# Optimization experiments

Hardware: AMD Instinct MI355X
Metric: run time of the kernel (lower is better)

## Reference

```python
import jax, jax.numpy as jnp
import numpy as np

B, S, D = 2, 2048, 2048
H, KV, HD = 8, 1, 256          # num_heads, num_kv_heads, head_dim
ROPE_BASE = 10000.0
NEG_INF = -1e9


def _rope_cos_sin(position_ids, head_dim, base):
    # position_ids: [B, S] -> cos/sin: [B, S, head_dim]
    inv_freq = 1.0 / (base ** (jnp.arange(0, head_dim, 2, dtype=jnp.float32) / head_dim))
    freqs = position_ids.astype(jnp.float32)[..., None] * inv_freq  # [B,S,HD/2]
    emb = jnp.concatenate([freqs, freqs], axis=-1)                  # [B,S,HD]
    return jnp.cos(emb), jnp.sin(emb)


def _rotate_half(x):
    h = x.shape[-1] // 2
    return jnp.concatenate([-x[..., h:], x[..., :h]], axis=-1)


def _apply_rope(x, cos, sin):
    # x: [B,h,S,HD]; cos/sin: [B,S,HD]
    c = cos[:, None, :, :]
    s = sin[:, None, :, :]
    return x * c + _rotate_half(x) * s


def setup_inputs() -> dict:
    key = jax.random.key(0)
    ks = jax.random.split(key, 6)
    hidden_state = jax.random.normal(ks[0], (B, S, D), dtype=jnp.float32)
    # additive causal mask: 0 on/below diagonal, -inf above
    causal = jnp.tril(jnp.ones((S, S), dtype=bool))
    attention_mask = jnp.where(causal, 0.0, NEG_INF).astype(jnp.float32)[None, None]  # [B?1,1,S,S]
    attention_mask = jnp.broadcast_to(attention_mask, (B, 1, S, S))
    position_ids = jnp.broadcast_to(jnp.arange(S, dtype=jnp.int64)[None, :], (B, S))
    scale = 0.02
    Wq = jax.random.normal(ks[1], (D, H * HD), dtype=jnp.float32) * scale
    Wk = jax.random.normal(ks[2], (D, KV * HD), dtype=jnp.float32) * scale
    Wv = jax.random.normal(ks[3], (D, KV * HD), dtype=jnp.float32) * scale
    Wo = jax.random.normal(ks[4], (H * HD, D), dtype=jnp.float32) * scale
    return {"hidden_state": hidden_state, "attention_mask": attention_mask,
            "position_ids": position_ids, "Wq": Wq, "Wk": Wk, "Wv": Wv, "Wo": Wo}


def reference(hidden_state, attention_mask, position_ids, Wq, Wk, Wv, Wo):
    bsz, q_len, _ = hidden_state.shape
    n_rep = H // KV
    # projections
    q = (hidden_state @ Wq).reshape(bsz, q_len, H, HD).transpose(0, 2, 1, 3)   # [B,H,S,HD]
    k = (hidden_state @ Wk).reshape(bsz, q_len, KV, HD).transpose(0, 2, 1, 3)  # [B,KV,S,HD]
    v = (hidden_state @ Wv).reshape(bsz, q_len, KV, HD).transpose(0, 2, 1, 3)
    # RoPE
    cos, sin = _rope_cos_sin(position_ids, HD, ROPE_BASE)
    q = _apply_rope(q, cos, sin)
    k = _apply_rope(k, cos, sin)
    # GQA: repeat kv heads
    k = jnp.repeat(k, n_rep, axis=1)  # [B,H,S,HD]
    v = jnp.repeat(v, n_rep, axis=1)
    # eager attention with full score matrix (faithful to source)
    scores = jnp.einsum('bhqd,bhkd->bhqk', q, k) / jnp.sqrt(jnp.float32(HD))
    scores = scores + attention_mask
    attn = jax.nn.softmax(scores.astype(jnp.float32), axis=-1).astype(q.dtype)
    out = jnp.einsum('bhqk,bhkd->bhqd', attn, v)            # [B,H,S,HD]
    out = out.transpose(0, 2, 1, 3).reshape(bsz, q_len, H * HD)
    return out @ Wo
```

## Files before the change

kernel.cpp:

```cpp
#include <hip/hip_runtime.h>
#include <cstdint>
#include <cstddef>

#define B_   2
#define S_   2048
#define D_   2048
#define H_   8
#define HD_  256
#define M_   (B_ * S_)
#define NQ_  (H_ * HD_)
#define NKV_ 256

typedef unsigned short u16;
typedef __attribute__((ext_vector_type(8))) short short8v;
typedef __attribute__((ext_vector_type(4))) float f32x4;

__device__ __forceinline__ u16 f2bf_rn(float x) {
    unsigned int u = __float_as_uint(x);
    unsigned int r = u + 0x7FFFu + ((u >> 16) & 1u);
    return (u16)(r >> 16);
}
__device__ __forceinline__ float bf2f(u16 h) {
    return __uint_as_float(((unsigned int)h) << 16);
}

__device__ __forceinline__ void gll16(const u16* g, u16* l) {
    __builtin_amdgcn_global_load_lds(
        (const __attribute__((address_space(1))) void*)(g),
        (__attribute__((address_space(3))) void*)(l), 16, 0, 0);
}

__global__ __launch_bounds__(256) void split_kernel(const float* __restrict__ in,
                                                    u16* __restrict__ hi,
                                                    u16* __restrict__ lo)
{
    const size_t i = ((size_t)blockIdx.x * 256 + threadIdx.x) * 8;
    float4 v0 = *(const float4*)(in + i);
    float4 v1 = *(const float4*)(in + i + 4);
    float xs[8] = {v0.x, v0.y, v0.z, v0.w, v1.x, v1.y, v1.z, v1.w};
    unsigned int hv[4], lv[4];
#pragma unroll
    for (int k = 0; k < 4; ++k) {
        u16 h0 = f2bf_rn(xs[2 * k]);
        u16 h1 = f2bf_rn(xs[2 * k + 1]);
        u16 l0 = f2bf_rn(xs[2 * k] - bf2f(h0));
        u16 l1 = f2bf_rn(xs[2 * k + 1] - bf2f(h1));
        hv[k] = (unsigned int)h0 | ((unsigned int)h1 << 16);
        lv[k] = (unsigned int)l0 | ((unsigned int)l1 << 16);
    }
    *(uint4*)(hi + i) = make_uint4(hv[0], hv[1], hv[2], hv[3]);
    *(uint4*)(lo + i) = make_uint4(lv[0], lv[1], lv[2], lv[3]);
}

__global__ __launch_bounds__(256) void tsplit_kernel(const float* __restrict__ W,
                                                     u16* __restrict__ Th,
                                                     u16* __restrict__ Tl,
                                                     int K, int N)
{
    __shared__ float t[64][65];
    const int kt = blockIdx.x, nt = blockIdx.y;
    const int c4 = (threadIdx.x & 15) * 4;
    const int r  = threadIdx.x >> 4;

#pragma unroll
    for (int s = 0; s < 4; ++s) {
        const int kk = r + s * 16;
        float4 v = *(const float4*)(W + (size_t)(kt * 64 + kk) * N + nt * 64 + c4);
        t[kk][c4 + 0] = v.x;
        t[kk][c4 + 1] = v.y;
        t[kk][c4 + 2] = v.z;
        t[kk][c4 + 3] = v.w;
    }
    __syncthreads();
#pragma unroll
    for (int s = 0; s < 4; ++s) {
        const int nn = r + s * 16;
        unsigned int hv[2], lv[2];
#pragma unroll
        for (int p = 0; p < 2; ++p) {
            u16 h0, h1, l0, l1;
            float x0 = t[c4 + 2 * p][nn];
            float x1 = t[c4 + 2 * p + 1][nn];
            h0 = f2bf_rn(x0); l0 = f2bf_rn(x0 - bf2f(h0));
            h1 = f2bf_rn(x1); l1 = f2bf_rn(x1 - bf2f(h1));
            hv[p] = (unsigned int)h0 | ((unsigned int)h1 << 16);
            lv[p] = (unsigned int)l0 | ((unsigned int)l1 << 16);
        }
        u16* ph = Th + (size_t)(nt * 64 + nn) * K + kt * 64 + c4;
        u16* pl = Tl + (size_t)(nt * 64 + nn) * K + kt * 64 + c4;
        *(uint2*)ph = make_uint2(hv[0], hv[1]);
        *(uint2*)pl = make_uint2(lv[0], lv[1]);
    }
}

__device__ __forceinline__ void mfma_gemm_tile(
    const u16* __restrict__ Ah, const u16* __restrict__ Al,
    const u16* __restrict__ Bh, const u16* __restrict__ Bl,
    float* __restrict__ C, const int Kd, const int ldc,
    const int bm0, const int bn0)
{
    __shared__ u16 ldsAh[128 * 32];
    __shared__ u16 ldsAl[128 * 32];
    __shared__ u16 ldsBh[128 * 32];
    __shared__ u16 ldsBl[128 * 32];

    const int tid  = threadIdx.x;
    const int lane = tid & 63;
    const int w    = tid >> 6;
    const int wr   = w >> 1, wc = w & 1;

    const int srow = w * 32 + (lane >> 2);
    const int schk = (lane & 3) * 8;
    const u16* gAh = Ah + (size_t)(bm0 + srow) * Kd + schk;
    const u16* gAl = Al + (size_t)(bm0 + srow) * Kd + schk;
    const u16* gBh = Bh + (size_t)(bn0 + srow) * Kd + schk;
    const u16* gBl = Bl + (size_t)(bn0 + srow) * Kd + schk;

    f32x4 acc[4][4];
#pragma unroll
    for (int i = 0; i < 4; ++i)
#pragma unroll
        for (int j = 0; j < 4; ++j) acc[i][j] = (f32x4){0.f, 0.f, 0.f, 0.f};

    const int fr = lane & 15;
    const int kb = (lane >> 4) * 8;

    for (int k0 = 0; k0 < Kd; k0 += 32) {
        if (k0) __syncthreads();
#pragma unroll
        for (int c = 0; c < 2; ++c) {
            const size_t go = (size_t)(c * 16) * Kd + k0;
            const int lb = (w * 32 + c * 16) * 32;
            gll16(gAh + go, &ldsAh[lb]);
            gll16(gAl + go, &ldsAl[lb]);
            gll16(gBh + go, &ldsBh[lb]);
            gll16(gBl + go, &ldsBl[lb]);
        }
        __syncthreads();

        short8v a_h[4], a_l[4], b_h[4], b_l[4];
#pragma unroll
        for (int f = 0; f < 4; ++f) {
            const int ra = (wr * 64 + f * 16 + fr) * 32 + kb;
            const int rb = (wc * 64 + f * 16 + fr) * 32 + kb;
            a_h[f] = *(const short8v*)&ldsAh[ra];
            a_l[f] = *(const short8v*)&ldsAl[ra];
            b_h[f] = *(const short8v*)&ldsBh[rb];
            b_l[f] = *(const short8v*)&ldsBl[rb];
        }
#pragma unroll
        for (int i = 0; i < 4; ++i)
#pragma unroll
            for (int j = 0; j < 4; ++j) {
                acc[i][j] = __builtin_amdgcn_mfma_f32_16x16x32_bf16(a_h[i], b_h[j], acc[i][j], 0, 0, 0);
                acc[i][j] = __builtin_amdgcn_mfma_f32_16x16x32_bf16(a_h[i], b_l[j], acc[i][j], 0, 0, 0);
                acc[i][j] = __builtin_amdgcn_mfma_f32_16x16x32_bf16(a_l[i], b_h[j], acc[i][j], 0, 0, 0);
            }
    }

    const int cr = (lane >> 4) * 4;
    const int cc = lane & 15;
#pragma unroll
    for (int i = 0; i < 4; ++i)
#pragma unroll
        for (int j = 0; j < 4; ++j) {
#pragma unroll
            for (int r = 0; r < 4; ++r) {
                C[(size_t)(bm0 + wr * 64 + i * 16 + cr + r) * ldc
                  + (bn0 + wc * 64 + j * 16 + cc)] = acc[i][j][r];
            }
        }
}

__global__ __launch_bounds__(256, 2) void qkv_mfma_kernel(
    const u16* __restrict__ Xh, const u16* __restrict__ Xl,
    const u16* __restrict__ WqTh, const u16* __restrict__ WqTl,
    const u16* __restrict__ WkTh, const u16* __restrict__ WkTl,
    const u16* __restrict__ WvTh, const u16* __restrict__ WvTl,
    float* __restrict__ Qo, float* __restrict__ Ko, float* __restrict__ Vo)
{
    const int bn = blockIdx.x;
    const u16 *Bh, *Bl; float* C; int ldc, col0;
    if (bn < 16)      { Bh = WqTh; Bl = WqTl; C = Qo; ldc = NQ_;  col0 = bn * 128; }
    else if (bn < 18) { Bh = WkTh; Bl = WkTl; C = Ko; ldc = NKV_; col0 = (bn - 16) * 128; }
    else              { Bh = WvTh; Bl = WvTl; C = Vo; ldc = NKV_; col0 = (bn - 18) * 128; }
    mfma_gemm_tile(Xh, Xl, Bh, Bl, C, D_, ldc, blockIdx.y * 128, col0);
}

__global__ __launch_bounds__(256, 2) void out_mfma_kernel(
    const u16* __restrict__ Ch, const u16* __restrict__ Cl,
    const u16* __restrict__ WoTh, const u16* __restrict__ WoTl,
    float* __restrict__ Out)
{
    mfma_gemm_tile(Ch, Cl, WoTh, WoTl, Out, NQ_, D_, blockIdx.y * 128, blockIdx.x * 128);
}

__global__ __launch_bounds__(128) void rope_split_q_kernel(
    const float* __restrict__ Qw, u16* __restrict__ Qh, u16* __restrict__ Ql)
{
    const int row = blockIdx.x;
    const int d = threadIdx.x;
    const int s = row & (S_ - 1);

    const float expo = (float)(2 * d) / (float)HD_;
    const float inv_freq = 1.0f / powf(10000.0f, expo);
    float sn, c;
    sincosf((float)s * inv_freq, &sn, &c);

    const float* qr = Qw + (size_t)row * NQ_;
    u16* qhr = Qh + (size_t)row * NQ_;
    u16* qlr = Ql + (size_t)row * NQ_;
#pragma unroll
    for (int h = 0; h < H_; ++h) {
        float x0 = qr[h * HD_ + d];
        float x1 = qr[h * HD_ + d + 128];
        float y0 = x0 * c - x1 * sn;
        float y1 = x1 * c + x0 * sn;
        u16 h0 = f2bf_rn(y0), h1 = f2bf_rn(y1);
        qhr[h * HD_ + d]       = h0;
        qhr[h * HD_ + d + 128] = h1;
        qlr[h * HD_ + d]       = f2bf_rn(y0 - bf2f(h0));
        qlr[h * HD_ + d + 128] = f2bf_rn(y1 - bf2f(h1));
    }
}

__global__ __launch_bounds__(128) void rope_split_k_swz_kernel(
    const float* __restrict__ Kw, u16* __restrict__ Kh, u16* __restrict__ Kl)
{
    const int row = blockIdx.x;
    const int d = threadIdx.x;
    const int s = row & (S_ - 1);
    const int xm = row & 7;

    const float expo = (float)(2 * d) / (float)HD_;
    const float inv_freq = 1.0f / powf(10000.0f, expo);
    float sn, c;
    sincosf((float)s * inv_freq, &sn, &c);

    const float* kr = Kw + (size_t)row * HD_;
    float x0 = kr[d], x1 = kr[d + 128];
    float y0 = x0 * c - x1 * sn;
    float y1 = x1 * c + x0 * sn;
    u16 h0 = f2bf_rn(y0), h1 = f2bf_rn(y1);

    const int o0 = (((d >> 3) ^ xm) << 3) | (d & 7);
    const int o1 = ((((d + 128) >> 3) ^ xm) << 3) | (d & 7);
    Kh[(size_t)row * HD_ + o0] = h0;
    Kh[(size_t)row * HD_ + o1] = h1;
    Kl[(size_t)row * HD_ + o0] = f2bf_rn(y0 - bf2f(h0));
    Kl[(size_t)row * HD_ + o1] = f2bf_rn(y1 - bf2f(h1));
}

#define KVB_ 32
#define PBS_ 44

__global__ __launch_bounds__(256, 2) void attn_mfma_kernel(
    const u16* __restrict__ Qh, const u16* __restrict__ Ql,
    const u16* __restrict__ Kh, const u16* __restrict__ Kl,
    const u16* __restrict__ VtH, const u16* __restrict__ VtL,
    float* __restrict__ O)
{
    __shared__ u16 kvK[2 * 32 * 256];
    __shared__ u16 kvV[2 * 256 * 32];
    __shared__ u16 pb[2 * 64 * PBS_];

    const int tid = threadIdx.x;
    const int lane = tid & 63;
    const int w = tid >> 6;

    const int u = blockIdx.x & 255;
    const int pair = blockIdx.x >> 8;
    const int qt_base = u & 31;
    const int qt = pair ? (31 - qt_base) : qt_base;
    const int bh = (u >> 5) + pair * 8;
    const int b = bh >> 3, h = bh & 7;

    const int fr = lane & 15;
    const int kq = (lane >> 4);
    const int xm = fr & 7;

    short8v qfh[8], qfl[8];
    {
        const size_t qrow = (size_t)(b * S_ + qt * 64 + w * 16 + fr);
        const u16* ph = Qh + qrow * NQ_ + h * HD_ + kq * 8;
        const u16* pl = Ql + qrow * NQ_ + h * HD_ + kq * 8;
#pragma unroll
        for (int ks = 0; ks < 8; ++ks) {
            qfh[ks] = *(const short8v*)(ph + ks * 32);
            qfl[ks] = *(const short8v*)(pl + ks * 32);
        }
    }

    f32x4 oacc[16];
#pragma unroll
    for (int f = 0; f < 16; ++f) oacc[f] = (f32x4){0.f, 0.f, 0.f, 0.f};
    float m_i[4] = {-1e30f, -1e30f, -1e30f, -1e30f};
    float l_i[4] = {0.f, 0.f, 0.f, 0.f};

    const u16* ksrc[2] = {Kh + (size_t)b * S_ * HD_, Kl + (size_t)b * S_ * HD_};
    const u16* vsrc[2] = {VtH + (size_t)b * HD_ * S_, VtL + (size_t)b * HD_ * S_};

    const int k_rl = w * 8 + (lane >> 5) * 0;
    const int k_hi = (lane >> 5);
    const int k_ch = lane & 31;
    const int v_dl = w * 64 + (lane >> 2);
    const int v_cc = (lane & 3) * 8;

    const int nkt = (qt + 1) * 2;

#define STAGE_K(KT)                                                            \
    {                                                                          \
        _Pragma("unroll")                                                      \
        for (int c = 0; c < 2; ++c) {                                          \
            _Pragma("unroll")                                                  \
            for (int t = 0; t < 4; ++t) {                                      \
                const int rl = k_rl + t * 2 + k_hi;                            \
                gll16(ksrc[c] + (size_t)((KT) * KVB_ + rl) * HD_ + k_ch * 8,   \
                      &kvK[c * 8192 + (w * 2048 + t * 512)]);                  \
            }                                                                  \
        }                                                                      \
    }

#define STAGE_V(KT)                                                            \
    {                                                                          \
        _Pragma("unroll")                                                      \
        for (int c = 0; c < 2; ++c) {                                          \
            _Pragma("unroll")                                                  \
            for (int t = 0; t < 4; ++t) {                                      \
                gll16(vsrc[c] + (size_t)(v_dl + t * 16) * S_ + (KT) * KVB_ + v_cc, \
                      &kvV[c * 8192 + (w * 2048 + t * 512)]);                  \
            }                                                                  \
        }                                                                      \
    }

    STAGE_K(0)
    STAGE_V(0)
    __syncthreads();

    for (int kt = 0; kt < nkt; ++kt) {
        const bool more = (kt + 1 < nkt);

        f32x4 s0 = (f32x4){0.f, 0.f, 0.f, 0.f};
        f32x4 s1 = (f32x4){0.f, 0.f, 0.f, 0.f};
#pragma unroll
        for (int ks = 0; ks < 8; ++ks) {
            const int ch = (ks * 4 + kq) ^ xm;
            short8v kh0 = *(const short8v*)&kvK[fr * 256 + ch * 8];
            short8v kh1 = *(const short8v*)&kvK[(16 + fr) * 256 + ch * 8];
            short8v kl0 = *(const short8v*)&kvK[8192 + fr * 256 + ch * 8];
            short8v kl1 = *(const short8v*)&kvK[8192 + (16 + fr) * 256 + ch * 8];
            s0 = __builtin_amdgcn_mfma_f32_16x16x32_bf16(qfh[ks], kh0, s0, 0, 0, 0);
            s1 = __builtin_amdgcn_mfma_f32_16x16x32_bf16(qfh[ks], kh1, s1, 0, 0, 0);
            s0 = __builtin_amdgcn_mfma_f32_16x16x32_bf16(qfh[ks], kl0, s0, 0, 0, 0);
            s1 = __builtin_amdgcn_mfma_f32_16x16x32_bf16(qfh[ks], kl1, s1, 0, 0, 0);
            s0 = __builtin_amdgcn_mfma_f32_16x16x32_bf16(qfl[ks], kh0, s0, 0, 0, 0);
            s1 = __builtin_amdgcn_mfma_f32_16x16x32_bf16(qfl[ks], kh1, s1, 0, 0, 0);
        }

        const int qglob = qt * 64 + w * 16 + kq * 4;
        const int kg = kt * KVB_ + fr;
        float mxv[4];
        bool need = false;
#pragma unroll
        for (int r = 0; r < 4; ++r) {
            float x0 = s0[r] * 0.0625f;
            float x1 = s1[r] * 0.0625f;
            if (kg > qglob + r)      x0 = -1e30f;
            if (kg + 16 > qglob + r) x1 = -1e30f;
            s0[r] = x0; s1[r] = x1;
            float mx = fmaxf(x0, x1);
#pragma unroll
            for (int off = 1; off < 16; off <<= 1)
                mx = fmaxf(mx, __shfl_xor(mx, off, 64));
            mxv[r] = mx;
            need = need || (mx > m_i[r] + 8.0f);
        }
        if (__any((int)need)) {
#pragma unroll
            for (int r = 0; r < 4; ++r) {
                const float mnew = fmaxf(m_i[r], mxv[r]);
                const float alpha = __expf(m_i[r] - mnew);
                l_i[r] *= alpha;
                m_i[r] = mnew;
#pragma unroll
                for (int f = 0; f < 16; ++f) oacc[f][r] *= alpha;
            }
        }
#pragma unroll
        for (int r = 0; r < 4; ++r) {
            const float p0 = __expf(s0[r] - m_i[r]);
            const float p1 = __expf(s1[r] - m_i[r]);
            float ps = p0 + p1;
#pragma unroll
            for (int off = 1; off < 16; off <<= 1)
                ps += __shfl_xor(ps, off, 64);
            l_i[r] += ps;

            const int prow = (w * 16 + kq * 4 + r) * PBS_;
            u16 h0 = f2bf_rn(p0), h1 = f2bf_rn(p1);
            pb[prow + fr]                    = h0;
            pb[prow + 16 + fr]               = h1;
            pb[64 * PBS_ + prow + fr]        = f2bf_rn(p0 - bf2f(h0));
            pb[64 * PBS_ + prow + 16 + fr]   = f2bf_rn(p1 - bf2f(h1));
        }
        __syncthreads();

        if (more) STAGE_K(kt + 1)

        {
            short8v pah = *(const short8v*)&pb[(w * 16 + fr) * PBS_ + kq * 8];
            short8v pal = *(const short8v*)&pb[64 * PBS_ + (w * 16 + fr) * PBS_ + kq * 8];
#pragma unroll
            for (int f = 0; f < 16; ++f) {
                const int vrow = (f * 16 + fr) * 32 + kq * 8;
                short8v vh = *(const short8v*)&kvV[vrow];
                short8v vl = *(const short8v*)&kvV[8192 + vrow];
                oacc[f] = __builtin_amdgcn_mfma_f32_16x16x32_bf16(pah, vh, oacc[f], 0, 0, 0);
                oacc[f] = __builtin_amdgcn_mfma_f32_16x16x32_bf16(pal, vh, oacc[f], 0, 0, 0);
                oacc[f] = __builtin_amdgcn_mfma_f32_16x16x32_bf16(pah, vl, oacc[f], 0, 0, 0);
            }
        }
        if (more) {
            __syncthreads();
            STAGE_V(kt + 1)
        }
    }

    float* orow = O + (size_t)(b * S_ + qt * 64 + w * 16 + kq * 4) * NQ_ + h * HD_ + fr;
#pragma unroll
    for (int r = 0; r < 4; ++r) {
        const float inv_l = 1.0f / l_i[r];
#pragma unroll
        for (int f = 0; f < 16; ++f)
            orow[(size_t)r * NQ_ + f * 16] = oacc[f][r] * inv_l;
    }
#undef STAGE_K
#undef STAGE_V
}

extern "C" void kernel_launch(void* const* d_in, const int* in_sizes, int n_in,
                              void* d_out, int out_size, void* d_ws, size_t ws_size,
                              hipStream_t stream)
{
    (void)in_sizes; (void)n_in; (void)out_size; (void)ws_size;

    const float* hidden = (const float*)d_in[0];
    const float* Wq = (const float*)d_in[3];
    const float* Wk = (const float*)d_in[4];
    const float* Wv = (const float*)d_in[5];
    const float* Wo = (const float*)d_in[6];
    float* out = (float*)d_out;

    char* ws = (char*)d_ws;
    float* Qw = (float*)(ws + 0);
    u16* Kh2 = (u16*)(ws + 0);
    u16* Kl2 = (u16*)(ws + 2097152u);
    u16* VtH = (u16*)(ws + 4194304u);
    u16* VtL = (u16*)(ws + 6291456u);
    float* Kw = (float*)(ws + 33554432u);
    float* Vw = (float*)(ws + 37748736u);
    float* Cw = (float*)(ws + 41943040u);
    u16* Ah  = (u16*)(ws + 75497472u);
    u16* Al  = (u16*)(ws + 92274688u);
    u16* WqTh = (u16*)(ws + 109051904u);
    u16* WqTl = (u16*)(ws + 117440512u);
    u16* WkTh = (u16*)(ws + 125829120u);
    u16* WkTl = (u16*)(ws + 126877696u);
    u16* WvTh = (u16*)(ws + 127926272u);
    u16* WvTl = (u16*)(ws + 128974848u);
    u16* WoTh = WqTh;
    u16* WoTl = WqTl;
    u16* Qhb = Ah;
    u16* Qlb = Al;

    split_kernel<<<dim3((M_ * D_) / (256 * 8)), dim3(256), 0, stream>>>(hidden, Ah, Al);

    tsplit_kernel<<<dim3(D_ / 64, NQ_ / 64),  dim3(256), 0, stream>>>(Wq, WqTh, WqTl, D_, NQ_);
    tsplit_kernel<<<dim3(D_ / 64, NKV_ / 64), dim3(256), 0, stream>>>(Wk, WkTh, WkTl, D_, NKV_);
    tsplit_kernel<<<dim3(D_ / 64, NKV_ / 64), dim3(256), 0, stream>>>(Wv, WvTh, WvTl, D_, NKV_);

    qkv_mfma_kernel<<<dim3(20, M_ / 128), dim3(256), 0, stream>>>(
        Ah, Al, WqTh, WqTl, WkTh, WkTl, WvTh, WvTl, Qw, Kw, Vw);

    rope_split_q_kernel<<<dim3(M_), dim3(128), 0, stream>>>(Qw, Qhb, Qlb);
    rope_split_k_swz_kernel<<<dim3(M_), dim3(128), 0, stream>>>(Kw, Kh2, Kl2);

    tsplit_kernel<<<dim3(S_ / 64, NKV_ / 64), dim3(256), 0, stream>>>(
        Vw, VtH, VtL, S_, NKV_);
    tsplit_kernel<<<dim3(S_ / 64, NKV_ / 64), dim3(256), 0, stream>>>(
        Vw + (size_t)S_ * NKV_, VtH + (size_t)HD_ * S_, VtL + (size_t)HD_ * S_, S_, NKV_);

    attn_mfma_kernel<<<dim3(512), dim3(256), 0, stream>>>(
        Qhb, Qlb, Kh2, Kl2, VtH, VtL, Cw);

    split_kernel<<<dim3((M_ * NQ_) / (256 * 8)), dim3(256), 0, stream>>>(Cw, Ah, Al);

    tsplit_kernel<<<dim3(NQ_ / 64, D_ / 64), dim3(256), 0, stream>>>(Wo, WoTh, WoTl, NQ_, D_);

    out_mfma_kernel<<<dim3(D_ / 128, M_ / 128), dim3(256), 0, stream>>>(
        Ah, Al, WoTh, WoTl, out);
}
```

Measured before the change: 603.0 us.

## Persistent attention with atomic work queue, fused bf16 split output, lazy max reduction

The attention kernel becomes persistent: 256 blocks pull (query-tile, batch-head) items from a global atomic counter, longest causal tiles first, to balance the triangular workload. The counter is reset inside the K-rope kernel. The attention epilogue now writes the hi/lo bf16 split of its output directly, which removes the separate split kernel and the fp32 context round-trip. The row-max shuffle reduction now runs only when some lane needs a rescale. The trade-offs are an extra barrier and atomic per work item, and reduced occupancy if two blocks per CU do not fit.

New measurement: 579.2 us. -4.0%, faster.

```diff
diff --git a/kernel.cpp b/kernel.cpp
--- a/kernel.cpp
+++ b/kernel.cpp
@@ -225,8 +225,11 @@
 }
 
 __global__ __launch_bounds__(128) void rope_split_k_swz_kernel(
-    const float* __restrict__ Kw, u16* __restrict__ Kh, u16* __restrict__ Kl)
-{
+    const float* __restrict__ Kw, u16* __restrict__ Kh, u16* __restrict__ Kl,
+    int* __restrict__ wq)
+{
+    if (blockIdx.x == 0 && threadIdx.x == 0) *wq = 0;
+
     const int row = blockIdx.x;
     const int d = threadIdx.x;
     const int s = row & (S_ - 1);
@@ -253,189 +256,204 @@
 
 #define KVB_ 32
 #define PBS_ 44
+#define NITEM_ 512
 
 __global__ __launch_bounds__(256, 2) void attn_mfma_kernel(
     const u16* __restrict__ Qh, const u16* __restrict__ Ql,
     const u16* __restrict__ Kh, const u16* __restrict__ Kl,
     const u16* __restrict__ VtH, const u16* __restrict__ VtL,
-    float* __restrict__ O)
+    u16* __restrict__ Ch, u16* __restrict__ Cl,
+    int* __restrict__ wq)
 {
     __shared__ u16 kvK[2 * 32 * 256];
     __shared__ u16 kvV[2 * 256 * 32];
     __shared__ u16 pb[2 * 64 * PBS_];
+    __shared__ int s_item;
 
     const int tid = threadIdx.x;
     const int lane = tid & 63;
     const int w = tid >> 6;
 
-    const int u = blockIdx.x & 255;
-    const int pair = blockIdx.x >> 8;
-    const int qt_base = u & 31;
-    const int qt = pair ? (31 - qt_base) : qt_base;
-    const int bh = (u >> 5) + pair * 8;
-    const int b = bh >> 3, h = bh & 7;
-
     const int fr = lane & 15;
     const int kq = (lane >> 4);
     const int xm = fr & 7;
 
-    short8v qfh[8], qfl[8];
-    {
-        const size_t qrow = (size_t)(b * S_ + qt * 64 + w * 16 + fr);
-        const u16* ph = Qh + qrow * NQ_ + h * HD_ + kq * 8;
-        const u16* pl = Ql + qrow * NQ_ + h * HD_ + kq * 8;
-#pragma unroll
-        for (int ks = 0; ks < 8; ++ks) {
-            qfh[ks] = *(const short8v*)(ph + ks * 32);
-            qfl[ks] = *(const short8v*)(pl + ks * 32);
-        }
-    }
-
-    f32x4 oacc[16];
-#pragma unroll
-    for (int f = 0; f < 16; ++f) oacc[f] = (f32x4){0.f, 0.f, 0.f, 0.f};
-    float m_i[4] = {-1e30f, -1e30f, -1e30f, -1e30f};
-    float l_i[4] = {0.f, 0.f, 0.f, 0.f};
-
-    const u16* ksrc[2] = {Kh + (size_t)b * S_ * HD_, Kl + (size_t)b * S_ * HD_};
-    const u16* vsrc[2] = {VtH + (size_t)b * HD_ * S_, VtL + (size_t)b * HD_ * S_};
-
-    const int k_rl = w * 8 + (lane >> 5) * 0;
     const int k_hi = (lane >> 5);
     const int k_ch = lane & 31;
     const int v_dl = w * 64 + (lane >> 2);
     const int v_cc = (lane & 3) * 8;
 
-    const int nkt = (qt + 1) * 2;
+    while (true) {
+        __syncthreads();
+        if (tid == 0) s_item = atomicAdd(wq, 1);
+        __syncthreads();
+        const int item = s_item;
+        if (item >= NITEM_) break;
+
+        const int qt = 31 - (item >> 4);
+        const int bh = item & 15;
+        const int b = bh >> 3, h = bh & 7;
+
+        short8v qfh[8], qfl[8];
+        {
+            const size_t qrow = (size_t)(b * S_ + qt * 64 + w * 16 + fr);
+            const u16* ph = Qh + qrow * NQ_ + h * HD_ + kq * 8;
+            const u16* pl = Ql + qrow * NQ_ + h * HD_ + kq * 8;
+#pragma unroll
+            for (int ks = 0; ks < 8; ++ks) {
+                qfh[ks] = *(const short8v*)(ph + ks * 32);
+                qfl[ks] = *(const short8v*)(pl + ks * 32);
+            }
+        }
+
+        f32x4 oacc[16];
+#pragma unroll
+        for (int f = 0; f < 16; ++f) oacc[f] = (f32x4){0.f, 0.f, 0.f, 0.f};
+        float m_i[4] = {-1e30f, -1e30f, -1e30f, -1e30f};
+        float l_i[4] = {0.f, 0.f, 0.f, 0.f};
+
+        const u16* ksrc[2] = {Kh + (size_t)b * S_ * HD_, Kl + (size_t)b * S_ * HD_};
+        const u16* vsrc[2] = {VtH + (size_t)b * HD_ * S_, VtL + (size_t)b * HD_ * S_};
+
+        const int nkt = (qt + 1) * 2;
 
 #define STAGE_K(KT)                                                            \
-    {                                                                          \
-        _Pragma("unroll")                                                      \
-        for (int c = 0; c < 2; ++c) {                                          \
+        {                                                                      \
             _Pragma("unroll")                                                  \
-            for (int t = 0; t < 4; ++t) {                                      \
-                const int rl = k_rl + t * 2 + k_hi;                            \
-                gll16(ksrc[c] + (size_t)((KT) * KVB_ + rl) * HD_ + k_ch * 8,   \
-                      &kvK[c * 8192 + (w * 2048 + t * 512)]);                  \
+            for (int c = 0; c < 2; ++c) {                                      \
+                _Pragma("unroll")                                              \
+                for (int t = 0; t < 4; ++t) {                                  \
+                    const int rl = w * 8 + t * 2 + k_hi;                       \
+                    gll16(ksrc[c] + (size_t)((KT) * KVB_ + rl) * HD_ + k_ch * 8, \
+                          &kvK[c * 8192 + (w * 2048 + t * 512)]);              \
+                }                                                              \
             }                                                                  \
-        }                                                                      \
-    }
+        }
 
 #define STAGE_V(KT)                                                            \
-    {                                                                          \
-        _Pragma("unroll")                                                      \
-        for (int c = 0; c < 2; ++c) {                                          \
+        {                                                                      \
             _Pragma("unroll")                                                  \
-            for (int t = 0; t < 4; ++t) {                                      \
-                gll16(vsrc[c] + (size_t)(v_dl + t * 16) * S_ + (KT) * KVB_ + v_cc, \
-                      &kvV[c * 8192 + (w * 2048 + t * 512)]);                  \
+            for (int c = 0; c < 2; ++c) {                                      \
+                _Pragma("unroll")                                              \
+                for (int t = 0; t < 4; ++t) {                                  \
+                    gll16(vsrc[c] + (size_t)(v_dl + t * 16) * S_ + (KT) * KVB_ + v_cc, \
+                          &kvV[c * 8192 + (w * 2048 + t * 512)]);              \
+                }                                                              \
             }                                                                  \
-        }                                                                      \
-    }
-
-    STAGE_K(0)
-    STAGE_V(0)
-    __syncthreads();
-
-    for (int kt = 0; kt < nkt; ++kt) {
-        const bool more = (kt + 1 < nkt);
-
-        f32x4 s0 = (f32x4){0.f, 0.f, 0.f, 0.f};
-        f32x4 s1 = (f32x4){0.f, 0.f, 0.f, 0.f};
-#pragma unroll
-        for (int ks = 0; ks < 8; ++ks) {
-            const int ch = (ks * 4 + kq) ^ xm;
-            short8v kh0 = *(const short8v*)&kvK[fr * 256 + ch * 8];
-            short8v kh1 = *(const short8v*)&kvK[(16 + fr) * 256 + ch * 8];
-            short8v kl0 = *(const short8v*)&kvK[8192 + fr * 256 + ch * 8];
-            short8v kl1 = *(const short8v*)&kvK[8192 + (16 + fr) * 256 + ch * 8];
-            s0 = __builtin_amdgcn_mfma_f32_16x16x32_bf16(qfh[ks], kh0, s0, 0, 0, 0);
-            s1 = __builtin_amdgcn_mfma_f32_16x16x32_bf16(qfh[ks], kh1, s1, 0, 0, 0);
-            s0 = __builtin_amdgcn_mfma_f32_16x16x32_bf16(qfh[ks], kl0, s0, 0, 0, 0);
-            s1 = __builtin_amdgcn_mfma_f32_16x16x32_bf16(qfh[ks], kl1, s1, 0, 0, 0);
-            s0 = __builtin_amdgcn_mfma_f32_16x16x32_bf16(qfl[ks], kh0, s0, 0, 0, 0);
-            s1 = __builtin_amdgcn_mfma_f32_16x16x32_bf16(qfl[ks], kh1, s1, 0, 0, 0);
-        }
-
-        const int qglob = qt * 64 + w * 16 + kq * 4;
-        const int kg = kt * KVB_ + fr;
-        float mxv[4];
-        bool need = false;
-#pragma unroll
-        for (int r = 0; r < 4; ++r) {
-            float x0 = s0[r] * 0.0625f;
-            float x1 = s1[r] * 0.0625f;
-            if (kg > qglob + r)      x0 = -1e30f;
-            if (kg + 16 > qglob + r) x1 = -1e30f;
-            s0[r] = x0; s1[r] = x1;
-            float mx = fmaxf(x0, x1);
-#pragma unroll
-            for (int off = 1; off < 16; off <<= 1)
-                mx = fmaxf(mx, __shfl_xor(mx, off, 64));
-            mxv[r] = mx;
-            need = need || (mx > m_i[r] + 8.0f);
-        }
-        if (__any((int)need)) {
+        }
+
+        STAGE_K(0)
+        STAGE_V(0)
+        __syncthreads();
+
+        for (int kt = 0; kt < nkt; ++kt) {
+            const bool more = (kt + 1 < nkt);
+
+            f32x4 s0 = (f32x4){0.f, 0.f, 0.f, 0.f};
+            f32x4 s1 = (f32x4){0.f, 0.f, 0.f, 0.f};
+#pragma unroll
+            for (int ks = 0; ks < 8; ++ks) {
+                const int ch = (ks * 4 + kq) ^ xm;
+                short8v kh0 = *(const short8v*)&kvK[fr * 256 + ch * 8];
+                short8v kh1 = *(const short8v*)&kvK[(16 + fr) * 256 + ch * 8];
+                short8v kl0 = *(const short8v*)&kvK[8192 + fr * 256 + ch * 8];
+                short8v kl1 = *(const short8v*)&kvK[8192 + (16 + fr) * 256 + ch * 8];
+                s0 = __builtin_amdgcn_mfma_f32_16x16x32_bf16(qfh[ks], kh0, s0, 0, 0, 0);
+                s1 = __builtin_amdgcn_mfma_f32_16x16x32_bf16(qfh[ks], kh1, s1, 0, 0, 0);
+                s0 = __builtin_amdgcn_mfma_f32_16x16x32_bf16(qfh[ks], kl0, s0, 0, 0, 0);
+                s1 = __builtin_amdgcn_mfma_f32_16x16x32_bf16(qfh[ks], kl1, s1, 0, 0, 0);
+                s0 = __builtin_amdgcn_mfma_f32_16x16x32_bf16(qfl[ks], kh0, s0, 0, 0, 0);
+                s1 = __builtin_amdgcn_mfma_f32_16x16x32_bf16(qfl[ks], kh1, s1, 0, 0, 0);
+            }
+
+            const int qglob = qt * 64 + w * 16 + kq * 4;
+            const int kg = kt * KVB_ + fr;
+            float x0v[4], x1v[4], mxl[4];
+            bool needl = false;
 #pragma unroll
             for (int r = 0; r < 4; ++r) {
-                const float mnew = fmaxf(m_i[r], mxv[r]);
-                const float alpha = __expf(m_i[r] - mnew);
-                l_i[r] *= alpha;
-                m_i[r] = mnew;
-#pragma unroll
-                for (int f = 0; f < 16; ++f) oacc[f][r] *= alpha;
-            }
-        }
-#pragma unroll
-        for (int r = 0; r < 4; ++r) {
-            const float p0 = __expf(s0[r] - m_i[r]);
-            const float p1 = __expf(s1[r] - m_i[r]);
-            float ps = p0 + p1;
-#pragma unroll
-            for (int off = 1; off < 16; off <<= 1)
-                ps += __shfl_xor(ps, off, 64);
-            l_i[r] += ps;
-
-            const int prow = (w * 16 + kq * 4 + r) * PBS_;
-            u16 h0 = f2bf_rn(p0), h1 = f2bf_rn(p1);
-            pb[prow + fr]                    = h0;
-            pb[prow + 16 + fr]               = h1;
-            pb[64 * PBS_ + prow + fr]        = f2bf_rn(p0 - bf2f(h0));
-            pb[64 * PBS_ + prow + 16 + fr]   = f2bf_rn(p1 - bf2f(h1));
-        }
-        __syncthreads();
-
-        if (more) STAGE_K(kt + 1)
+                float x0 = s0[r] * 0.0625f;
+                float x1 = s1[r] * 0.0625f;
+                if (kg > qglob + r)      x0 = -1e30f;
+                if (kg + 16 > qglob + r) x1 = -1e30f;
+                x0v[r] = x0; x1v[r] = x1;
+                mxl[r] = fmaxf(x0, x1);
+                needl = needl || (mxl[r] > m_i[r] + 8.0f);
+            }
+            if (__any((int)needl)) {
+#pragma unroll
+                for (int r = 0; r < 4; ++r) {
+                    float mx = mxl[r];
+#pragma unroll
+                    for (int off = 1; off < 16; off <<= 1)
+                        mx = fmaxf(mx, __shfl_xor(mx, off, 64));
+                    const float mnew = fmaxf(m_i[r], mx);
+                    const float alpha = __expf(m_i[r] - mnew);
+                    l_i[r] *= alpha;
+                    m_i[r] = mnew;
+#pragma unroll
+                    for (int f = 0; f < 16; ++f) oacc[f][r] *= alpha;
+                }
+            }
+#pragma unroll
+            for (int r = 0; r < 4; ++r) {
+                const float p0 = __expf(x0v[r] - m_i[r]);
+                const float p1 = __expf(x1v[r] - m_i[r]);
+                float ps = p0 + p1;
+#pragma unroll
+                for (int off = 1; off < 16; off <<= 1)
+                    ps += __shfl_xor(ps, off, 64);
+                l_i[r] += ps;
+
+                const int prow = (w * 16 + kq * 4 + r) * PBS_;
+                u16 h0 = f2bf_rn(p0), h1 = f2bf_rn(p1);
+                pb[prow + fr]                    = h0;
+                pb[prow + 16 + fr]               = h1;
+                pb[64 * PBS_ + prow + fr]        = f2bf_rn(p0 - bf2f(h0));
+                pb[64 * PBS_ + prow + 16 + fr]   = f2bf_rn(p1 - bf2f(h1));
+            }
+            __syncthreads();
+
+            if (more) STAGE_K(kt + 1)
+
+            {
+                short8v pah = *(const short8v*)&pb[(w * 16 + fr) * PBS_ + kq * 8];
+                short8v pal = *(const short8v*)&pb[64 * PBS_ + (w * 16 + fr) * PBS_ + kq * 8];
+#pragma unroll
+                for (int f = 0; f < 16; ++f) {
+                    const int vrow = (f * 16 + fr) * 32 + kq * 8;
+                    short8v vh = *(const short8v*)&kvV[vrow];
+                    short8v vl = *(const short8v*)&kvV[8192 + vrow];
+                    oacc[f] = __builtin_amdgcn_mfma_f32_16x16x32_bf16(pah, vh, oacc[f], 0, 0, 0);
+                    oacc[f] = __builtin_amdgcn_mfma_f32_16x16x32_bf16(pal, vh, oacc[f], 0, 0, 0);
+                    oacc[f] = __builtin_amdgcn_mfma_f32_16x16x32_bf16(pah, vl, oacc[f], 0, 0, 0);
+                }
+            }
+            if (more) {
+                __syncthreads();
+                STAGE_V(kt + 1)
+            }
+        }
 
         {
-            short8v pah = *(const short8v*)&pb[(w * 16 + fr) * PBS_ + kq * 8];
-            short8v pal = *(const short8v*)&pb[64 * PBS_ + (w * 16 + fr) * PBS_ + kq * 8];
-#pragma unroll
-            for (int f = 0; f < 16; ++f) {
-                const int vrow = (f * 16 + fr) * 32 + kq * 8;
-                short8v vh = *(const short8v*)&kvV[vrow];
-                short8v vl = *(const short8v*)&kvV[8192 + vrow];
-                oacc[f] = __builtin_amdgcn_mfma_f32_16x16x32_bf16(pah, vh, oacc[f], 0, 0, 0);
-                oacc[f] = __builtin_amdgcn_mfma_f32_16x16x32_bf16(pal, vh, oacc[f], 0, 0, 0);
-                oacc[f] = __builtin_amdgcn_mfma_f32_16x16x32_bf16(pah, vl, oacc[f], 0, 0, 0);
-            }
-        }
-        if (more) {
-            __syncthreads();
-            STAGE_V(kt + 1)
-        }
-    }
-
-    float* orow = O + (size_t)(b * S_ + qt * 64 + w * 16 + kq * 4) * NQ_ + h * HD_ + fr;
-#pragma unroll
-    for (int r = 0; r < 4; ++r) {
-        const float inv_l = 1.0f / l_i[r];
-#pragma unroll
-        for (int f = 0; f < 16; ++f)
-            orow[(size_t)r * NQ_ + f * 16] = oacc[f][r] * inv_l;
-    }
+            const size_t obase = (size_t)(b * S_ + qt * 64 + w * 16 + kq * 4) * NQ_ + h * HD_ + fr;
+            u16* ohr = Ch + obase;
+            u16* olr = Cl + obase;
+#pragma unroll
+            for (int r = 0; r < 4; ++r) {
+                const float inv_l = 1.0f / l_i[r];
+#pragma unroll
+                for (int f = 0; f < 16; ++f) {
+                    const float v = oacc[f][r] * inv_l;
+                    const u16 hh = f2bf_rn(v);
+                    ohr[(size_t)r * NQ_ + f * 16] = hh;
+                    olr[(size_t)r * NQ_ + f * 16] = f2bf_rn(v - bf2f(hh));
+                }
+            }
+        }
 #undef STAGE_K
 #undef STAGE_V
+    }
 }
 
 extern "C" void kernel_launch(void* const* d_in, const int* in_sizes, int n_in,
@@ -457,9 +475,11 @@
     u16* Kl2 = (u16*)(ws + 2097152u);
     u16* VtH = (u16*)(ws + 4194304u);
     u16* VtL = (u16*)(ws + 6291456u);
+    int* wq  = (int*)(ws + 8388608u);
     float* Kw = (float*)(ws + 33554432u);
     float* Vw = (float*)(ws + 37748736u);
-    float* Cw = (float*)(ws + 41943040u);
+    u16* Ch2 = (u16*)(ws + 41943040u);
+    u16* Cl2 = (u16*)(ws + 58720256u);
     u16* Ah  = (u16*)(ws + 75497472u);
     u16* Al  = (u16*)(ws + 92274688u);
     u16* WqTh = (u16*)(ws + 109051904u);
@@ -483,20 +503,18 @@
         Ah, Al, WqTh, WqTl, WkTh, WkTl, WvTh, WvTl, Qw, Kw, Vw);
 
     rope_split_q_kernel<<<dim3(M_), dim3(128), 0, stream>>>(Qw, Qhb, Qlb);
-    rope_split_k_swz_kernel<<<dim3(M_), dim3(128), 0, stream>>>(Kw, Kh2, Kl2);
+    rope_split_k_swz_kernel<<<dim3(M_), dim3(128), 0, stream>>>(Kw, Kh2, Kl2, wq);
 
     tsplit_kernel<<<dim3(S_ / 64, NKV_ / 64), dim3(256), 0, stream>>>(
         Vw, VtH, VtL, S_, NKV_);
     tsplit_kernel<<<dim3(S_ / 64, NKV_ / 64), dim3(256), 0, stream>>>(
         Vw + (size_t)S_ * NKV_, VtH + (size_t)HD_ * S_, VtL + (size_t)HD_ * S_, S_, NKV_);
 
-    attn_mfma_kernel<<<dim3(512), dim3(256), 0, stream>>>(
-        Qhb, Qlb, Kh2, Kl2, VtH, VtL, Cw);
-
-    split_kernel<<<dim3((M_ * NQ_) / (256 * 8)), dim3(256), 0, stream>>>(Cw, Ah, Al);
+    attn_mfma_kernel<<<dim3(256), dim3(256), 0, stream>>>(
+        Qhb, Qlb, Kh2, Kl2, VtH, VtL, Ch2, Cl2, wq);
 
     tsplit_kernel<<<dim3(NQ_ / 64, D_ / 64), dim3(256), 0, stream>>>(Wo, WoTh, WoTl, NQ_, D_);
 
     out_mfma_kernel<<<dim3(D_ / 128, M_ / 128), dim3(256), 0, stream>>>(
-        Ah, Al, WoTh, WoTl, out);
-}
+        Ch2, Cl2, WoTh, WoTl, out);
+}
```
